# Kernel optimization log

Hardware: AMD Instinct MI355X
Metric: run time of the kernel (lower is better)

## Reference

```python
import jax, jax.numpy as jnp
import numpy as np
from math import exp, log

# Instant-NGP style multi-hash-grid constants (match init_kwargs)
BASE_RES = 16
MAX_RES = 2048
N_GRIDS = 16
LOG2_T = 19
TABLE_SIZE = 1 << LOG2_T  # power of two -> mod == low-bit mask
FEAT = 2
N_POINTS = 1_000_000

_pls = exp((log(MAX_RES) - log(BASE_RES)) / (N_GRIDS - 1))
RESOLUTIONS = np.floor(np.array([BASE_RES * _pls ** i for i in range(N_GRIDS)])).astype(np.float32)
# 8 voxel corner offsets, i-major (i*4 + j*2 + k) like the torch VOXEL_VTX_OFFSET
OFFSETS = np.array([[i, j, k] for i in (0, 1) for j in (0, 1) for k in (0, 1)], dtype=np.int32)
PRIMES = np.array([1, 2654435761, 805459861], dtype=np.uint32)


def setup_inputs() -> dict:
    key = jax.random.key(0)
    k1, k2 = jax.random.split(key)
    x = jax.random.normal(k1, (N_POINTS, 3), dtype=jnp.float32)
    # nn.init.uniform_(weight, a=-1e-4, b=1e-4)
    tables = jax.random.uniform(k2, (N_GRIDS, TABLE_SIZE, FEAT),
                                minval=-1e-4, maxval=1e-4, dtype=jnp.float32)
    return {"x": x, "tables": tables}


def _forward(x, tables):
    inbox = jnp.all((x >= -1.0) & (x <= 1.0), axis=-1)  # [B]
    offs = jnp.asarray(OFFSETS)                          # [8,3]
    primes = jnp.asarray(PRIMES)                         # [3] uint32
    res = jnp.asarray(RESOLUTIONS)                       # [G]
    # torch computes x_normed / interp weights under no_grad -> no grad to x
    xs = jax.lax.stop_gradient(x)

    def level(table, r):
        # (x - bbox_min) / (bbox_max - bbox_min) * resolution, bbox = [-1,1]^3
        xn = (xs + 1.0) * 0.5 * r                        # [B,3]
        v0 = jnp.floor(xn).astype(jnp.int32)             # [B,3]
        w = xn - v0.astype(jnp.float32)                  # [B,3] trilerp weights
        vidx = (v0[:, None, :] + offs[None]).astype(jnp.uint32)  # [B,8,3]
        # prime-XOR spatial hash; uint32 wraparound matches torch int64 math
        # modulo the power-of-two table size (low bits identical)
        h = (vidx[..., 0] * primes[0]) ^ (vidx[..., 1] * primes[1]) ^ (vidx[..., 2] * primes[2])
        h = (h & jnp.uint32(TABLE_SIZE - 1)).astype(jnp.int32)   # [B,8]
        feats = table[h]                                  # [B,8,F] gather
        # corner (i,j,k) weight = prod over dims of (w if bit else 1-w)
        wgt = jnp.prod(jnp.where(offs[None] == 1, w[:, None, :], 1.0 - w[:, None, :]), axis=-1)  # [B,8]
        c = jnp.einsum('bc,bcf->bf', wgt, feats)          # [B,F]
        return jnp.where(inbox[:, None], c, 0.0)          # out-of-bbox -> zeros

    per_level = jax.vmap(level)(tables, res)              # [G,B,F]
    B = x.shape[0]
    return jnp.transpose(per_level, (1, 0, 2)).reshape(B, N_GRIDS * FEAT)


def reference(x, tables):
    return _forward(x, tables)
```

## Files before the change

kernel.cpp:

```cpp
#include <hip/hip_runtime.h>
#include <hip/hip_bf16.h>
#include <math.h>

#define N_POINTS 1000000
#define N_GRIDS  16
#define LOG2_T   19
#define TABLE_MASK ((1u << LOG2_T) - 1u)
#define NBLOCKS  ((N_POINTS + 255) / 256)
#define CONV_BLOCKS 4096
#define FUSED_BLOCKS 2048
#define TAILB_BLOCKS 4096
#define N_ENTRIES (N_GRIDS << LOG2_T)
#define NCELL_AX 32
#define N_CELLS  (NCELL_AX * NCELL_AX * NCELL_AX)

struct ResArr { float r[N_GRIDS]; };

__device__ __forceinline__ unsigned pack_bf16x2(float a, float b)
{
    __hip_bfloat16 ha = __float2bfloat16(a);
    __hip_bfloat16 hb = __float2bfloat16(b);
    unsigned short ua = *(unsigned short*)&ha;
    unsigned short ub = *(unsigned short*)&hb;
    return (unsigned)ua | ((unsigned)ub << 16);
}

__device__ __forceinline__ float2 unpack_bf16x2(unsigned v)
{
    unsigned lo = (v & 0xffffu) << 16;
    unsigned hi = v & 0xffff0000u;
    return make_float2(__uint_as_float(lo), __uint_as_float(hi));
}

__device__ __forceinline__ unsigned expand_bits(unsigned v)
{
    v &= 0x3ffu;
    v = (v | (v << 16)) & 0x30000FFu;
    v = (v | (v << 8))  & 0x300F00Fu;
    v = (v | (v << 4))  & 0x30C30C3u;
    v = (v | (v << 2))  & 0x9249249u;
    return v;
}

__device__ __forceinline__ int morton_cell(float x0, float x1, float x2)
{
    int cx = (int)floorf((x0 + 1.f) * 16.f);
    int cy = (int)floorf((x1 + 1.f) * 16.f);
    int cz = (int)floorf((x2 + 1.f) * 16.f);
    cx = min(NCELL_AX - 1, max(0, cx));
    cy = min(NCELL_AX - 1, max(0, cy));
    cz = min(NCELL_AX - 1, max(0, cz));
    return (int)((expand_bits((unsigned)cx) << 2) |
                 (expand_bits((unsigned)cy) << 1) |
                  expand_bits((unsigned)cz));
}

__device__ __forceinline__ void gather_level_bf16(
    float x0, float x1, float x2, float r,
    const unsigned* __restrict__ tbl, float& c0, float& c1)
{
    const float xn0 = (x0 + 1.0f) * 0.5f * r;
    const float xn1 = (x1 + 1.0f) * 0.5f * r;
    const float xn2 = (x2 + 1.0f) * 0.5f * r;
    const float f0 = floorf(xn0), f1 = floorf(xn1), f2 = floorf(xn2);
    const unsigned v0 = (unsigned)(int)f0;
    const unsigned v1 = (unsigned)(int)f1;
    const unsigned v2 = (unsigned)(int)f2;
    const float w0 = xn0 - f0, w1 = xn1 - f1, w2 = xn2 - f2;

    unsigned fv[8];
    #pragma unroll
    for (int k = 0; k < 8; ++k) {
        const unsigned vx = v0 + ((k >> 2) & 1);
        const unsigned vy = v1 + ((k >> 1) & 1);
        const unsigned vz = v2 + (k & 1);
        unsigned h = vx ^ (vy * 2654435761u) ^ (vz * 805459861u);
        fv[k] = tbl[h & TABLE_MASK];
    }
    c0 = 0.f; c1 = 0.f;
    #pragma unroll
    for (int k = 0; k < 8; ++k) {
        const float wgt = ((k & 4) ? w0 : 1.0f - w0) *
                          ((k & 2) ? w1 : 1.0f - w1) *
                          ((k & 1) ? w2 : 1.0f - w2);
        const float2 f = unpack_bf16x2(fv[k]);
        c0 += wgt * f.x;
        c1 += wgt * f.y;
    }
}

__global__ __launch_bounds__(256)
void hist_kernel(const float* __restrict__ x, int* __restrict__ rank,
                 unsigned* __restrict__ hist)
{
    const int p = blockIdx.x * 256 + threadIdx.x;
    if (p >= N_POINTS) return;
    const float x0 = x[3 * p], x1 = x[3 * p + 1], x2 = x[3 * p + 2];
    const bool inbox = (x0 >= -1.f) & (x0 <= 1.f) &
                       (x1 >= -1.f) & (x1 <= 1.f) &
                       (x2 >= -1.f) & (x2 <= 1.f);
    if (inbox) {
        const int cell = morton_cell(x0, x1, x2);
        atomicAdd(&hist[cell], 1u);
        rank[p] = cell;
    } else {
        rank[p] = -1;
    }
}

__global__ __launch_bounds__(1024)
void scan_kernel(unsigned* __restrict__ hist, unsigned* __restrict__ counter)
{
    __shared__ unsigned partial[1024];
    const int tid = threadIdx.x;
    uint4* __restrict__ hp = (uint4*)hist + tid * 8;
    uint4 vv[8];
    unsigned s = 0;
    #pragma unroll
    for (int i = 0; i < 8; ++i) {
        vv[i] = hp[i];
        s += vv[i].x + vv[i].y + vv[i].z + vv[i].w;
    }
    partial[tid] = s;
    __syncthreads();
    for (int off = 1; off < 1024; off <<= 1) {
        unsigned t = (tid >= off) ? partial[tid - off] : 0u;
        __syncthreads();
        partial[tid] += t;
        __syncthreads();
    }
    if (tid == 1023) counter[0] = partial[1023];
    unsigned run = partial[tid] - s;
    #pragma unroll
    for (int i = 0; i < 8; ++i) {
        uint4 o;
        o.x = run; run += vv[i].x;
        o.y = run; run += vv[i].y;
        o.z = run; run += vv[i].z;
        o.w = run; run += vv[i].w;
        hp[i] = o;
    }
}

__global__ __launch_bounds__(256)
void scatter_conv_kernel(const float* __restrict__ tables,
                         unsigned* __restrict__ tb,
                         const float* __restrict__ x, int* __restrict__ rank,
                         float4* __restrict__ xw, unsigned* __restrict__ hist)
{
    if (blockIdx.x < CONV_BLOCKS) {
        const unsigned nthr = CONV_BLOCKS * 256;
        for (unsigned e4 = blockIdx.x * 256 + threadIdx.x; e4 < (N_ENTRIES / 4);
             e4 += nthr) {
            const float4 a = ((const float4*)tables)[2 * e4];
            const float4 b = ((const float4*)tables)[2 * e4 + 1];
            uint4 o;
            o.x = pack_bf16x2(a.x, a.y);
            o.y = pack_bf16x2(a.z, a.w);
            o.z = pack_bf16x2(b.x, b.y);
            o.w = pack_bf16x2(b.z, b.w);
            ((uint4*)tb)[e4] = o;
        }
    } else {
        const int p = (blockIdx.x - CONV_BLOCKS) * 256 + threadIdx.x;
        if (p >= N_POINTS) return;
        const int cell = rank[p];
        if (cell < 0) return;
        const unsigned rk = atomicAdd(&hist[cell], 1u);
        rank[p] = (int)rk;
        xw[rk] = make_float4(x[3 * p], x[3 * p + 1], x[3 * p + 2],
                             __int_as_float(p));
    }
}

__global__ __launch_bounds__(256)
void fused_levels_kernel(const float4* __restrict__ xw,
                         const unsigned* __restrict__ counter,
                         const unsigned* __restrict__ tb,
                         unsigned* __restrict__ ws2, ResArr res)
{
    const unsigned k   = blockIdx.x & 7;
    const unsigned bix = blockIdx.x >> 3;
    const unsigned nbx = gridDim.x >> 3;
    const unsigned cnt = *counter;

    auto b8 = [&](unsigned e) {
        return (unsigned)(((unsigned long long)e * cnt) >> 3);
    };

    const unsigned per = (2 * cnt + nbx - 1) / nbx;
    const unsigned blo = bix * per;
    const unsigned bhi = blo + per;

    unsigned cum = 0;
    #pragma unroll 1
    for (int tix = 0; tix < 16; ++tix) {
        int g; unsigned e;
        if (tix < 7) { g = tix; e = k; }
        else {
            const unsigned u = 9u * k + (unsigned)(tix - 7);
            g = 7 + (int)(u >> 3);
            e = u & 7u;
        }
        const unsigned lo = b8(e), hi = b8(e + 1);
        const unsigned len = hi - lo;
        const unsigned s0 = max(blo, cum);
        const unsigned s1 = min(bhi, cum + len);
        cum += len;
        if (s0 >= s1) continue;

        const float r = res.r[g];
        const unsigned* __restrict__ tbl = tb + ((size_t)g << LOG2_T);
        unsigned* __restrict__ wrow = ws2 + (size_t)g * N_POINTS;
        const unsigned ilo = lo + (s0 - (cum - len));
        const unsigned ihi = lo + (s1 - (cum - len));
        for (unsigned i = ilo + threadIdx.x; i < ihi; i += 256) {
            const float4 v = xw[i];
            float c0, c1;
            gather_level_bf16(v.x, v.y, v.z, r, tbl, c0, c1);
            wrow[i] = pack_bf16x2(c0, c1);
        }
    }
}

__global__ __launch_bounds__(256)
void tail_kernel(const int* __restrict__ rank, const float4* __restrict__ xw,
                 const unsigned* __restrict__ counter,
                 const unsigned* __restrict__ ws2, float* __restrict__ out)
{
    const int t = threadIdx.x;
    if (blockIdx.x < NBLOCKS) {
        const int P0 = blockIdx.x * 256;
        float4* __restrict__ out4 = (float4*)out + (size_t)P0 * 8;
        const float4 z = make_float4(0.f, 0.f, 0.f, 0.f);
        #pragma unroll
        for (int i = 0; i < 8; ++i) {
            const int j  = i * 256 + t;
            const int pp = P0 + (j >> 3);
            if (pp < N_POINTS && rank[pp] < 0) out4[j] = z;
        }
    } else {
        const unsigned cnt = *counter;
        const unsigned tot = cnt * 8u;
        const unsigned bix = blockIdx.x - NBLOCKS;
        for (unsigned tg = bix * 256 + t; tg < tot; tg += TAILB_BLOCKS * 256) {
            const unsigned i = tg >> 3, q = tg & 7;
            const unsigned a = ws2[(size_t)(2 * q) * N_POINTS + i];
            const unsigned b = ws2[(size_t)(2 * q + 1) * N_POINTS + i];
            const int p = __float_as_int(xw[i].w);
            const float2 fa = unpack_bf16x2(a);
            const float2 fb = unpack_bf16x2(b);
            ((float4*)out)[(size_t)p * 8 + q] =
                make_float4(fa.x, fa.y, fb.x, fb.y);
        }
    }
}

__device__ __forceinline__ void gather_level_f32(
    float x0, float x1, float x2, float r,
    const float2* __restrict__ tbl, float& c0, float& c1)
{
    const float xn0 = (x0 + 1.0f) * 0.5f * r;
    const float xn1 = (x1 + 1.0f) * 0.5f * r;
    const float xn2 = (x2 + 1.0f) * 0.5f * r;
    const float f0 = floorf(xn0), f1 = floorf(xn1), f2 = floorf(xn2);
    const unsigned v0 = (unsigned)(int)f0;
    const unsigned v1 = (unsigned)(int)f1;
    const unsigned v2 = (unsigned)(int)f2;
    const float w0 = xn0 - f0, w1 = xn1 - f1, w2 = xn2 - f2;
    c0 = 0.f; c1 = 0.f;
    #pragma unroll
    for (int k = 0; k < 8; ++k) {
        const unsigned vx = v0 + ((k >> 2) & 1);
        const unsigned vy = v1 + ((k >> 1) & 1);
        const unsigned vz = v2 + (k & 1);
        unsigned h = (vx * 1u) ^ (vy * 2654435761u) ^ (vz * 805459861u);
        h &= TABLE_MASK;
        const float wgt = ((k & 4) ? w0 : 1.0f - w0) *
                          ((k & 2) ? w1 : 1.0f - w1) *
                          ((k & 1) ? w2 : 1.0f - w2);
        const float2 f = tbl[h];
        c0 += wgt * f.x;
        c1 += wgt * f.y;
    }
}

__global__ __launch_bounds__(256)
void mono_kernel(const float* __restrict__ x, const float* __restrict__ tables,
                 float* __restrict__ out, ResArr res)
{
    int idx = blockIdx.x * blockDim.x + threadIdx.x;
    if (idx >= N_POINTS * N_GRIDS) return;
    int b = idx >> 4, g = idx & 15;
    float x0 = x[b * 3], x1 = x[b * 3 + 1], x2 = x[b * 3 + 2];
    bool inbox = (x0 >= -1.f) & (x0 <= 1.f) & (x1 >= -1.f) & (x1 <= 1.f) &
                 (x2 >= -1.f) & (x2 <= 1.f);
    float c0 = 0.f, c1 = 0.f;
    if (inbox) {
        const float2* tbl = (const float2*)tables + ((size_t)g << LOG2_T);
        gather_level_f32(x0, x1, x2, res.r[g], tbl, c0, c1);
    }
    ((float2*)out)[(size_t)b * N_GRIDS + g] = make_float2(c0, c1);
}

extern "C" void kernel_launch(void* const* d_in, const int* in_sizes, int n_in,
                              void* d_out, int out_size, void* d_ws, size_t ws_size,
                              hipStream_t stream)
{
    const float* x      = (const float*)d_in[0];
    const float* tables = (const float*)d_in[1];
    float* out          = (float*)d_out;

    ResArr res;
    double pls = exp((log(2048.0) - log(16.0)) / 15.0);
    for (int i = 0; i < N_GRIDS; ++i)
        res.r[i] = (float)floor(16.0 * pow(pls, (double)i));

    const size_t off_hist = 256;
    const size_t off_rank = off_hist + (size_t)N_CELLS * 4;
    const size_t off_xw   = off_rank + (size_t)N_POINTS * 4;
    const size_t off_ws2  = off_xw + (size_t)N_POINTS * 16;
    const size_t off_tb   = off_ws2 + (size_t)N_GRIDS * N_POINTS * 4;
    const size_t ws_needed = off_tb + (size_t)N_ENTRIES * 4;

    if (ws_size < ws_needed) {
        int total = N_POINTS * N_GRIDS;
        mono_kernel<<<(total + 255) / 256, 256, 0, stream>>>(x, tables, out, res);
        return;
    }

    char* w = (char*)d_ws;
    unsigned* counter = (unsigned*)w;
    unsigned* hist    = (unsigned*)(w + off_hist);
    int*      rank    = (int*)(w + off_rank);
    float4*   xw      = (float4*)(w + off_xw);
    unsigned* ws2     = (unsigned*)(w + off_ws2);
    unsigned* tb      = (unsigned*)(w + off_tb);

    (void)hipMemsetAsync(w, 0, off_rank, stream);
    hist_kernel<<<NBLOCKS, 256, 0, stream>>>(x, rank, hist);
    scan_kernel<<<1, 1024, 0, stream>>>(hist, counter);
    scatter_conv_kernel<<<CONV_BLOCKS + NBLOCKS, 256, 0, stream>>>(
        tables, tb, x, rank, xw, hist);
    fused_levels_kernel<<<FUSED_BLOCKS, 256, 0, stream>>>(xw, counter, tb,
                                                          ws2, res);
    tail_kernel<<<NBLOCKS + TAILB_BLOCKS, 256, 0, stream>>>(rank, xw, counter,
                                                            ws2, out);
}
```

Baseline: 207.7 us.

## Distribute level work in 64-point wavefront chunks with grid-stride scheduling

Replaces the per-block contiguous range split over (level, segment) tasks with a per-wavefront grid-stride loop over 64-point chunks. Thread 0 precomputes a small task table in shared memory, with segment boundaries aligned to 64 points. The aim is better load balance, no partial wavefronts at segment edges, and less per-thread index arithmetic. Chunks are now strided across wavefronts instead of contiguous per block, which could reduce locality of table accesses within a block and adds a __syncthreads.

After: 208.3 us. No clear change (+0.3%).

```diff
diff --git a/kernel.cpp b/kernel.cpp
--- a/kernel.cpp
+++ b/kernel.cpp
@@ -179,46 +179,54 @@
                          const unsigned* __restrict__ tb,
                          unsigned* __restrict__ ws2, ResArr res)
 {
+    __shared__ unsigned s_g[16], s_lo[16], s_hi[16], s_cum[17];
+    __shared__ float    s_r[16];
+
     const unsigned k   = blockIdx.x & 7;
     const unsigned bix = blockIdx.x >> 3;
     const unsigned nbx = gridDim.x >> 3;
     const unsigned cnt = *counter;
 
-    auto b8 = [&](unsigned e) {
-        return (unsigned)(((unsigned long long)e * cnt) >> 3);
-    };
-
-    const unsigned per = (2 * cnt + nbx - 1) / nbx;
-    const unsigned blo = bix * per;
-    const unsigned bhi = blo + per;
-
-    unsigned cum = 0;
-    #pragma unroll 1
-    for (int tix = 0; tix < 16; ++tix) {
-        int g; unsigned e;
-        if (tix < 7) { g = tix; e = k; }
-        else {
-            const unsigned u = 9u * k + (unsigned)(tix - 7);
-            g = 7 + (int)(u >> 3);
-            e = u & 7u;
-        }
-        const unsigned lo = b8(e), hi = b8(e + 1);
-        const unsigned len = hi - lo;
-        const unsigned s0 = max(blo, cum);
-        const unsigned s1 = min(bhi, cum + len);
-        cum += len;
-        if (s0 >= s1) continue;
-
-        const float r = res.r[g];
-        const unsigned* __restrict__ tbl = tb + ((size_t)g << LOG2_T);
-        unsigned* __restrict__ wrow = ws2 + (size_t)g * N_POINTS;
-        const unsigned ilo = lo + (s0 - (cum - len));
-        const unsigned ihi = lo + (s1 - (cum - len));
-        for (unsigned i = ilo + threadIdx.x; i < ihi; i += 256) {
+    if (threadIdx.x == 0) {
+        unsigned cum = 0;
+        for (int tix = 0; tix < 16; ++tix) {
+            unsigned g, e;
+            if (tix < 7) { g = (unsigned)tix; e = k; }
+            else {
+                const unsigned u = 9u * k + (unsigned)(tix - 7);
+                g = 7u + (u >> 3);
+                e = u & 7u;
+            }
+            const unsigned lo = (e == 0) ? 0u
+                : (unsigned)((((unsigned long long)e * cnt) >> 3) & ~63ull);
+            const unsigned hi = (e == 7) ? cnt
+                : (unsigned)((((unsigned long long)(e + 1) * cnt) >> 3) & ~63ull);
+            s_g[tix] = g; s_lo[tix] = lo; s_hi[tix] = hi;
+            s_cum[tix] = cum;
+            cum += (hi - lo + 63) >> 6;
+        }
+        s_cum[16] = cum;
+        for (int g = 0; g < 16; ++g) s_r[g] = res.r[g];
+    }
+    __syncthreads();
+
+    const unsigned lane  = threadIdx.x & 63;
+    const unsigned gw    = bix * 4 + (threadIdx.x >> 6);
+    const unsigned ngw   = nbx * 4;
+    const unsigned total = s_cum[16];
+
+    unsigned t = 0;
+    for (unsigned u = gw; u < total; u += ngw) {
+        while (u >= s_cum[t + 1]) ++t;
+        const unsigned g = s_g[t];
+        const unsigned i = s_lo[t] + ((u - s_cum[t]) << 6) + lane;
+        if (i < s_hi[t]) {
+            const float r = s_r[g];
+            const unsigned* __restrict__ tbl = tb + ((size_t)g << LOG2_T);
             const float4 v = xw[i];
             float c0, c1;
             gather_level_bf16(v.x, v.y, v.z, r, tbl, c0, c1);
-            wrow[i] = pack_bf16x2(c0, c1);
+            ws2[(size_t)g * N_POINTS + i] = pack_bf16x2(c0, c1);
         }
     }
 }
```
